# Kernel optimization log

Hardware: AMD Instinct MI355X
Metric: run time of the kernel (lower is better)

The kernel has to match this reference:

```python
import jax, jax.numpy as jnp
import numpy as np

D_MODEL = 1024
N_HEADS = 16
HEAD_DIM = D_MODEL // N_HEADS


def setup_inputs() -> dict:
    key = jax.random.key(0)
    ks = jax.random.split(key, 9)
    s = 1.0 / np.sqrt(D_MODEL)
    x = jax.random.normal(ks[0], (2, 2048, D_MODEL), dtype=jnp.float32)
    wq = jax.random.uniform(ks[1], (D_MODEL, D_MODEL), jnp.float32, -s, s)
    bq = jax.random.uniform(ks[2], (D_MODEL,), jnp.float32, -s, s)
    wk = jax.random.uniform(ks[3], (D_MODEL, D_MODEL), jnp.float32, -s, s)
    bk = jax.random.uniform(ks[4], (D_MODEL,), jnp.float32, -s, s)
    wv = jax.random.uniform(ks[5], (D_MODEL, D_MODEL), jnp.float32, -s, s)
    bv = jax.random.uniform(ks[6], (D_MODEL,), jnp.float32, -s, s)
    wo = jax.random.uniform(ks[7], (D_MODEL, D_MODEL), jnp.float32, -s, s)
    bo = jax.random.uniform(ks[8], (D_MODEL,), jnp.float32, -s, s)
    return {"x": x, "wq": wq, "bq": bq, "wk": wk, "bk": bk,
            "wv": wv, "bv": bv, "wo": wo, "bo": bo}


def reference(x, wq, bq, wk, bk, wv, bv, wo, bo):
    B, S, _ = x.shape
    scale = HEAD_DIM ** -0.5

    def proj(w, b):
        # torch Linear: x @ W^T + b, then split heads -> [B, H, S, Dh]
        y = jnp.einsum('bsd,ed->bse', x, w) + b
        return y.reshape(B, S, N_HEADS, HEAD_DIM).transpose(0, 2, 1, 3)

    q = proj(wq, bq)
    k = proj(wk, bk)
    v = proj(wv, bv)

    attn = jnp.einsum('bhqd,bhkd->bhqk', q, k) * scale  # [B,H,S,S]
    causal = jnp.triu(jnp.ones((S, S), dtype=bool), k=1)
    attn = jnp.where(causal, -jnp.inf, attn)
    attn = jax.nn.softmax(attn, axis=-1)
    out = jnp.einsum('bhqk,bhkd->bhqd', attn, v)
    out = out.transpose(0, 2, 1, 3).reshape(B, S, D_MODEL)
    return jnp.einsum('bsd,ed->bse', out, wo) + bo
```

## Files before the change

kernel.cpp:

```cpp
#include <hip/hip_runtime.h>
#include <hip/hip_bf16.h>

#define D_MODEL 1024
#define NHEADS  16
#define HDIM    64
#define SEQ     2048
#define BATCH   2
#define MROWS   (BATCH * SEQ)
#define CHELEM  ((size_t)BATCH * NHEADS * SEQ * HDIM)

typedef __bf16 bf16x8 __attribute__((ext_vector_type(8)));
typedef float  f32x4  __attribute__((ext_vector_type(4)));

__device__ __forceinline__ unsigned short f2bf(float f) {
  unsigned u = __builtin_bit_cast(unsigned, f);
  return (unsigned short)((u + 0x7fffu + ((u >> 16) & 1u)) >> 16);
}

__device__ __forceinline__ float fexp2(float x) {
#if __has_builtin(__builtin_amdgcn_exp2f)
  return __builtin_amdgcn_exp2f(x);
#else
  return __expf(x * 0.6931471805599453f);
#endif
}

__device__ __forceinline__ f32x4 mfma16(bf16x8 a, bf16x8 b, f32x4 c) {
  return __builtin_amdgcn_mfma_f32_16x16x32_bf16(a, b, c, 0, 0, 0);
}

__device__ __forceinline__ void gll16(const unsigned short* g, unsigned short* l) {
  __builtin_amdgcn_global_load_lds(
      (const __attribute__((address_space(1))) unsigned*)g,
      (__attribute__((address_space(3))) unsigned*)l, 16, 0, 0);
}

__global__ void cvt_f32_bf16(const float* __restrict__ in,
                             unsigned short* __restrict__ out, int n4) {
  int i = blockIdx.x * blockDim.x + threadIdx.x;
  if (i >= n4) return;
  float4 v = reinterpret_cast<const float4*>(in)[i];
  ushort4 o;
  o.x = f2bf(v.x); o.y = f2bf(v.y); o.z = f2bf(v.z); o.w = f2bf(v.w);
  reinterpret_cast<ushort4*>(out)[i] = o;
}

__global__ void cvt_w4(const float* __restrict__ s0, const float* __restrict__ s1,
                       const float* __restrict__ s2, const float* __restrict__ s3,
                       unsigned short* __restrict__ d0, unsigned short* __restrict__ d1,
                       unsigned short* __restrict__ d2, unsigned short* __restrict__ d3) {
  int i = blockIdx.x * blockDim.x + threadIdx.x;
  const int y = blockIdx.y;
  const float* s = (y == 0) ? s0 : (y == 1) ? s1 : (y == 2) ? s2 : s3;
  unsigned short* d = (y == 0) ? d0 : (y == 1) ? d1 : (y == 2) ? d2 : d3;
  float4 v = reinterpret_cast<const float4*>(s)[i];
  ushort4 o;
  o.x = f2bf(v.x); o.y = f2bf(v.y); o.z = f2bf(v.z); o.w = f2bf(v.w);
  reinterpret_cast<ushort4*>(d)[i] = o;
}

template <int MODE>
__global__ __launch_bounds__(256) void gemm_bt2(
    const unsigned short* __restrict__ A,
    const unsigned short* __restrict__ Bt,
    const float* __restrict__ b0, const float* __restrict__ b1,
    const float* __restrict__ b2,
    void* __restrict__ outp, int M, int N, int K) {
  __shared__ __align__(16) unsigned short lA[128 * 32];
  __shared__ __align__(16) unsigned short lB[128 * 32];
  const int tid = threadIdx.x;
  const int m0 = blockIdx.y * 128, n0 = blockIdx.x * 128;
  const int lane = tid & 63, wid = tid >> 6;
  const int wr = wid >> 1, wc = wid & 1;
  const int fr = lane & 15, g = lane >> 4;

  const int srow = wid * 32 + (lane >> 2);
  const int scol = (lane & 3) * 8;
  const unsigned short* gA = A + (size_t)(m0 + srow) * K + scol;
  const unsigned short* gB = Bt + (size_t)(n0 + srow) * K + scol;
  unsigned short* lAw = lA + wid * 1024;
  unsigned short* lBw = lB + wid * 1024;

  f32x4 acc[4][4];
#pragma unroll
  for (int i = 0; i < 4; ++i)
#pragma unroll
    for (int j = 0; j < 4; ++j) acc[i][j] = (f32x4){0.f, 0.f, 0.f, 0.f};

  for (int kt = 0; kt < K; kt += 32) {
    gll16(gA + kt, lAw);
    gll16(gA + (size_t)16 * K + kt, lAw + 512);
    gll16(gB + kt, lBw);
    gll16(gB + (size_t)16 * K + kt, lBw + 512);
    __syncthreads();
    bf16x8 af[4], bfv[4];
#pragma unroll
    for (int i = 0; i < 4; ++i)
      af[i] = *reinterpret_cast<const bf16x8*>(
          &lA[(wr * 64 + i * 16 + fr) * 32 + g * 8]);
#pragma unroll
    for (int j = 0; j < 4; ++j)
      bfv[j] = *reinterpret_cast<const bf16x8*>(
          &lB[(wc * 64 + j * 16 + fr) * 32 + g * 8]);
#pragma unroll
    for (int i = 0; i < 4; ++i)
#pragma unroll
      for (int j = 0; j < 4; ++j)
        acc[i][j] = mfma16(af[i], bfv[j], acc[i][j]);
    __syncthreads();
  }

  const int src = n0 >> 10;
  const float* bp = (MODE == 2) ? b0 : (src == 0 ? b0 : (src == 1 ? b1 : b2));
#pragma unroll
  for (int i = 0; i < 4; ++i)
#pragma unroll
    for (int j = 0; j < 4; ++j)
#pragma unroll
      for (int r = 0; r < 4; ++r) {
        int m = m0 + wr * 64 + i * 16 + g * 4 + r;
        int n = n0 + wc * 64 + j * 16 + fr;
        if (MODE == 2) {
          float val = acc[i][j][r] + bp[n];
          reinterpret_cast<float*>(outp)[(size_t)m * N + n] = val;
        } else {
          int within = n & 1023;
          float val = acc[i][j][r] + bp[within];
          if (src == 0) val *= 0.1803368867f;
          int b = m >> 11, s = m & 2047;
          int hh = within >> 6, dh = within & 63;
          size_t idx;
          if (src != 2)
            idx = ((size_t)(b * NHEADS + hh) * SEQ + s) * HDIM + dh;
          else
            idx = ((size_t)(b * NHEADS + hh) * HDIM + dh) * SEQ + s;
          reinterpret_cast<unsigned short*>(outp)[(size_t)src * CHELEM + idx] =
              f2bf(val);
        }
      }
}

__global__ __launch_bounds__(256) void attn_fwd10(
    const unsigned short* __restrict__ Q,
    const unsigned short* __restrict__ Km,
    const unsigned short* __restrict__ Vt,
    unsigned short* __restrict__ O) {
  const int tid = threadIdx.x;
  const int lane = tid & 63, wid = tid >> 6;
  const int fr = lane & 15, g = lane >> 4;
  const int lin = blockIdx.x;
  const int c = lin & 7;
  const int t = lin >> 3;
  const int j = t & 15;
  const int sgrp = t >> 4;
  const int slab = sgrp * 8 + c;
  const int b = slab >> 4, h = slab & 15;
  const int bh = b * NHEADS + h;

  __shared__ __align__(16) unsigned short lK[2][4096];
  __shared__ __align__(16) unsigned short lV[2][4096];
  __shared__ __align__(16) char plf[4][16 * 272];
  char* plw = plf[wid];

  const unsigned short* kptr = Km + (size_t)bh * SEQ * HDIM;
  const unsigned short* vptr = Vt + (size_t)bh * HDIM * SEQ;

  const int sr0 = tid >> 3;
  const int sch = tid & 7;
  const int schx = ((sch ^ (sr0 & 7)) << 3);
  const int kswz0 = ((g ^ (fr & 7)) << 3);
  const int kswz1 = (((4 + g) ^ (fr & 7)) << 3);

#define STAGE(BI, N0)                                                       \
  { gll16(kptr + (size_t)((N0) + sr0) * HDIM + schx, &lK[BI][wid * 512]);   \
    gll16(kptr + (size_t)((N0) + sr0 + 32) * HDIM + schx,                   \
          &lK[BI][2048 + wid * 512]);                                       \
    gll16(vptr + (size_t)sr0 * SEQ + (N0) + schx, &lV[BI][wid * 512]);      \
    gll16(vptr + (size_t)(sr0 + 32) * SEQ + (N0) + schx,                    \
          &lV[BI][2048 + wid * 512]); }

#pragma unroll 1
  for (int pass = 0; pass < 2; ++pass) {
    const int qt = pass ? (124 - 4 * j + wid) : (4 * j + wid);
    const int q0 = qt * 16;
    const int nkt = pass ? (32 - j) : (j + 1);

    const unsigned short* qb = Q + ((size_t)bh * SEQ + q0 + fr) * HDIM + g * 8;
    bf16x8 qa0 = *reinterpret_cast<const bf16x8*>(qb);
    bf16x8 qa1 = *reinterpret_cast<const bf16x8*>(qb + 32);

    f32x4 oacc[4];
#pragma unroll
    for (int i = 0; i < 4; ++i) oacc[i] = (f32x4){0.f, 0.f, 0.f, 0.f};
    float mreg[4] = {-3e30f, -3e30f, -3e30f, -3e30f};
    float lrow[4] = {0.f, 0.f, 0.f, 0.f};
    float mtile = -3e30f;

    STAGE(0, 0);
    __syncthreads();

    for (int kt = 0; kt < nkt; ++kt) {
      const int bi = kt & 1;
      if (kt + 1 < nkt) STAGE(bi ^ 1, (kt + 1) * 64);
      const int n0 = kt * 64;
      bf16x8 kf0[4], kf1[4];
#pragma unroll
      for (int cc = 0; cc < 4; ++cc) {
        kf0[cc] = *reinterpret_cast<const bf16x8*>(
            &lK[bi][(cc * 16 + fr) * 64 + kswz0]);
        kf1[cc] = *reinterpret_cast<const bf16x8*>(
            &lK[bi][(cc * 16 + fr) * 64 + kswz1]);
      }
      f32x4 s[4];
#pragma unroll
      for (int cc = 0; cc < 4; ++cc) {
        s[cc] = (f32x4){0.f, 0.f, 0.f, 0.f};
        s[cc] = mfma16(qa0, kf0[cc], s[cc]);
        s[cc] = mfma16(qa1, kf1[cc], s[cc]);
      }
      float sv[4][4];
      float lmax = -3e30f;
      if (kt == nkt - 1) {
#pragma unroll
        for (int cc = 0; cc < 4; ++cc)
#pragma unroll
          for (int r = 0; r < 4; ++r) {
            sv[cc][r] = (n0 + cc * 16 + fr <= q0 + g * 4 + r) ? s[cc][r]
                                                              : -1e30f;
            lmax = fmaxf(lmax, sv[cc][r]);
          }
      } else {
#pragma unroll
        for (int cc = 0; cc < 4; ++cc)
#pragma unroll
          for (int r = 0; r < 4; ++r) {
            sv[cc][r] = s[cc][r];
            lmax = fmaxf(lmax, sv[cc][r]);
          }
      }
      if (!__all(lmax - mtile <= 11.5f)) {
#pragma unroll
        for (int r = 0; r < 4; ++r) {
          float tm = fmaxf(fmaxf(sv[0][r], sv[1][r]), fmaxf(sv[2][r], sv[3][r]));
#pragma unroll
          for (int msk = 1; msk < 16; msk <<= 1)
            tm = fmaxf(tm, __shfl_xor(tm, msk, 64));
          const float mn = fmaxf(mreg[r], tm);
          const float al = fexp2(mreg[r] - mn);
          mreg[r] = mn;
          lrow[r] *= al;
#pragma unroll
          for (int nf = 0; nf < 4; ++nf) oacc[nf][r] *= al;
        }
        mtile = fminf(fminf(mreg[0], mreg[1]), fminf(mreg[2], mreg[3]));
      }
#pragma unroll
      for (int r = 0; r < 4; ++r) {
        const int rl = g * 4 + r;
#pragma unroll
        for (int cc = 0; cc < 4; ++cc) {
          float p = fexp2(sv[cc][r] - mreg[r]);
          lrow[r] += p;
          *reinterpret_cast<float*>(plw + rl * 272 + (cc * 16 + fr) * 4) = p;
        }
      }
#pragma unroll
      for (int blk = 0; blk < 2; ++blk) {
        const int abase = fr * 272 + blk * 128 + g * 32;
        f32x4 lo = *reinterpret_cast<const f32x4*>(plw + abase);
        f32x4 hi = *reinterpret_cast<const f32x4*>(plw + abase + 16);
        union { __bf16 e[8]; bf16x8 v; } cu;
#pragma unroll
        for (int t2 = 0; t2 < 4; ++t2) {
          cu.e[t2] = (__bf16)lo[t2];
          cu.e[4 + t2] = (__bf16)hi[t2];
        }
        bf16x8 pa = cu.v;
        const int vs = blk ? kswz1 : kswz0;
#pragma unroll
        for (int nf = 0; nf < 4; ++nf) {
          bf16x8 vfr = *reinterpret_cast<const bf16x8*>(
              &lV[bi][(nf * 16 + fr) * 64 + vs]);
          oacc[nf] = mfma16(pa, vfr, oacc[nf]);
        }
      }
      __syncthreads();
    }

#pragma unroll
    for (int r = 0; r < 4; ++r) {
      float ls = lrow[r];
#pragma unroll
      for (int msk = 1; msk < 16; msk <<= 1) ls += __shfl_xor(ls, msk, 64);
      const float inv = 1.f / ls;
      const size_t base =
          ((size_t)b * SEQ + q0 + g * 4 + r) * D_MODEL + h * HDIM;
#pragma unroll
      for (int nf = 0; nf < 4; ++nf)
        O[base + nf * 16 + fr] = f2bf(oacc[nf][r] * inv);
    }
  }
#undef STAGE
}

extern "C" void kernel_launch(void* const* d_in, const int* in_sizes, int n_in,
                              void* d_out, int out_size, void* d_ws,
                              size_t ws_size, hipStream_t stream) {
  const float* x  = (const float*)d_in[0];
  const float* wq = (const float*)d_in[1];
  const float* bq = (const float*)d_in[2];
  const float* wk = (const float*)d_in[3];
  const float* bk = (const float*)d_in[4];
  const float* wv = (const float*)d_in[5];
  const float* bv = (const float*)d_in[6];
  const float* wo = (const float*)d_in[7];
  const float* bo = (const float*)d_in[8];
  float* out = (float*)d_out;

  char* w = (char*)d_ws;
  unsigned short* xb    = (unsigned short*)w; w += (size_t)MROWS * D_MODEL * 2;
  unsigned short* wqkvb = (unsigned short*)w; w += (size_t)3 * D_MODEL * D_MODEL * 2;
  unsigned short* wob   = (unsigned short*)w; w += (size_t)D_MODEL * D_MODEL * 2;
  unsigned short* Qb    = (unsigned short*)w; w += CHELEM * 2 * 3;
  unsigned short* Ob    = (unsigned short*)w; w += (size_t)MROWS * D_MODEL * 2;
  unsigned short* Kb  = Qb + CHELEM;
  unsigned short* Vtb = Qb + 2 * CHELEM;

  {
    int n4 = MROWS * D_MODEL / 4;
    cvt_f32_bf16<<<n4 / 256, 256, 0, stream>>>(x, xb, n4);
  }
  {
    int n4 = D_MODEL * D_MODEL / 4;
    cvt_w4<<<dim3(n4 / 256, 4), 256, 0, stream>>>(
        wq, wk, wv, wo, wqkvb, wqkvb + (size_t)D_MODEL * D_MODEL,
        wqkvb + (size_t)2 * D_MODEL * D_MODEL, wob);
  }

  gemm_bt2<3><<<dim3(3 * D_MODEL / 128, MROWS / 128), 256, 0, stream>>>(
      xb, wqkvb, bq, bk, bv, Qb, MROWS, 3 * D_MODEL, D_MODEL);

  attn_fwd10<<<512, 256, 0, stream>>>(Qb, Kb, Vtb, Ob);

  gemm_bt2<2><<<dim3(D_MODEL / 128, MROWS / 128), 256, 0, stream>>>(
      Ob, wob, bo, bo, bo, out, MROWS, D_MODEL, D_MODEL);
}
```

Before: 132.5 us.

## Fuse both causal query passes into one KV sweep and store P as bf16

The two sequential passes over K/V, one for an early query tile and one for the mirrored late tile, become a single loop. Both tiles share each staged K/V block, so the early tile's K/V blocks are loaded once instead of twice. V fragments are hoisted into registers and reused by both tiles. The probability scratch now holds swizzled bf16 instead of padded fp32, which shrinks LDS traffic and drops the repacking conversion. The cost is roughly double the accumulator and softmax register state, which may lower occupancy or cause spills.

```diff
diff --git a/kernel.cpp b/kernel.cpp
--- a/kernel.cpp
+++ b/kernel.cpp
@@ -140,7 +140,7 @@
       }
 }
 
-__global__ __launch_bounds__(256) void attn_fwd10(
+__global__ __launch_bounds__(256) void attn_fwd11(
     const unsigned short* __restrict__ Q,
     const unsigned short* __restrict__ Km,
     const unsigned short* __restrict__ Vt,
@@ -159,8 +159,10 @@
 
   __shared__ __align__(16) unsigned short lK[2][4096];
   __shared__ __align__(16) unsigned short lV[2][4096];
-  __shared__ __align__(16) char plf[4][16 * 272];
-  char* plw = plf[wid];
+  __shared__ __align__(16) unsigned short plA[4][1024];
+  __shared__ __align__(16) unsigned short plB[4][1024];
+  char* plwA = reinterpret_cast<char*>(plA[wid]);
+  char* plwB = reinterpret_cast<char*>(plB[wid]);
 
   const unsigned short* kptr = Km + (size_t)bh * SEQ * HDIM;
   const unsigned short* vptr = Vt + (size_t)bh * HDIM * SEQ;
@@ -179,128 +181,141 @@
     gll16(vptr + (size_t)(sr0 + 32) * SEQ + (N0) + schx,                    \
           &lV[BI][2048 + wid * 512]); }
 
-#pragma unroll 1
-  for (int pass = 0; pass < 2; ++pass) {
-    const int qt = pass ? (124 - 4 * j + wid) : (4 * j + wid);
-    const int q0 = qt * 16;
-    const int nkt = pass ? (32 - j) : (j + 1);
-
-    const unsigned short* qb = Q + ((size_t)bh * SEQ + q0 + fr) * HDIM + g * 8;
-    bf16x8 qa0 = *reinterpret_cast<const bf16x8*>(qb);
-    bf16x8 qa1 = *reinterpret_cast<const bf16x8*>(qb + 32);
-
-    f32x4 oacc[4];
-#pragma unroll
-    for (int i = 0; i < 4; ++i) oacc[i] = (f32x4){0.f, 0.f, 0.f, 0.f};
-    float mreg[4] = {-3e30f, -3e30f, -3e30f, -3e30f};
-    float lrow[4] = {0.f, 0.f, 0.f, 0.f};
-    float mtile = -3e30f;
-
-    STAGE(0, 0);
+#define QKSTEP(QA0, QA1, S)                                                 \
+  { _Pragma("unroll") for (int cc = 0; cc < 4; ++cc) {                      \
+      S[cc] = (f32x4){0.f, 0.f, 0.f, 0.f};                                  \
+      S[cc] = mfma16(QA0, kf0[cc], S[cc]);                                  \
+      S[cc] = mfma16(QA1, kf1[cc], S[cc]);                                  \
+    } }
+
+#define SMAXP(S, MREG, LROW, OACC, MTILE, PLW, Q0, ISLAST, N0)              \
+  { float sv[4][4];                                                         \
+    float lmax = -3e30f;                                                    \
+    if (ISLAST) {                                                           \
+      _Pragma("unroll") for (int cc = 0; cc < 4; ++cc)                      \
+      _Pragma("unroll") for (int r = 0; r < 4; ++r) {                       \
+        sv[cc][r] = ((N0) + cc * 16 + fr <= (Q0) + g * 4 + r) ? S[cc][r]    \
+                                                              : -1e30f;     \
+        lmax = fmaxf(lmax, sv[cc][r]);                                      \
+      }                                                                     \
+    } else {                                                                \
+      _Pragma("unroll") for (int cc = 0; cc < 4; ++cc)                      \
+      _Pragma("unroll") for (int r = 0; r < 4; ++r) {                       \
+        sv[cc][r] = S[cc][r];                                               \
+        lmax = fmaxf(lmax, sv[cc][r]);                                      \
+      }                                                                     \
+    }                                                                       \
+    if (!__all(lmax - MTILE <= 11.5f)) {                                    \
+      _Pragma("unroll") for (int r = 0; r < 4; ++r) {                       \
+        float tm = fmaxf(fmaxf(sv[0][r], sv[1][r]),                         \
+                         fmaxf(sv[2][r], sv[3][r]));                        \
+        _Pragma("unroll") for (int msk = 1; msk < 16; msk <<= 1)            \
+            tm = fmaxf(tm, __shfl_xor(tm, msk, 64));                        \
+        const float mn = fmaxf(MREG[r], tm);                                \
+        const float al = fexp2(MREG[r] - mn);                               \
+        MREG[r] = mn;                                                       \
+        LROW[r] *= al;                                                      \
+        _Pragma("unroll") for (int nf = 0; nf < 4; ++nf)                    \
+            OACC[nf][r] *= al;                                              \
+      }                                                                     \
+      MTILE = fminf(fminf(MREG[0], MREG[1]), fminf(MREG[2], MREG[3]));      \
+    }                                                                       \
+    _Pragma("unroll") for (int r = 0; r < 4; ++r) {                         \
+      const int rl = g * 4 + r;                                             \
+      _Pragma("unroll") for (int cc = 0; cc < 4; ++cc) {                    \
+        float p = fexp2(sv[cc][r] - MREG[r]);                               \
+        LROW[r] += p;                                                       \
+        int byte = (rl * 128 + (cc * 16 + fr) * 2) ^ ((rl & 7) << 4);       \
+        *reinterpret_cast<unsigned short*>((PLW) + byte) =                  \
+            __builtin_bit_cast(unsigned short, (__bf16)p);                  \
+      }                                                                     \
+    } }
+
+#define PVSTEP(PLW, OACC)                                                   \
+  { _Pragma("unroll") for (int blk = 0; blk < 2; ++blk) {                   \
+      int byte = (fr * 128 + blk * 64 + g * 16) ^ ((fr & 7) << 4);          \
+      bf16x8 pa = *reinterpret_cast<const bf16x8*>((PLW) + byte);           \
+      _Pragma("unroll") for (int nf = 0; nf < 4; ++nf)                      \
+          OACC[nf] = mfma16(pa, vfr[blk][nf], OACC[nf]);                    \
+    } }
+
+#define EPI(LROW, OACC, Q0)                                                 \
+  { _Pragma("unroll") for (int r = 0; r < 4; ++r) {                         \
+      float ls = LROW[r];                                                   \
+      _Pragma("unroll") for (int msk = 1; msk < 16; msk <<= 1)              \
+          ls += __shfl_xor(ls, msk, 64);                                    \
+      const float inv = 1.f / ls;                                           \
+      const size_t base =                                                   \
+          ((size_t)b * SEQ + (Q0) + g * 4 + r) * D_MODEL + h * HDIM;        \
+      _Pragma("unroll") for (int nf = 0; nf < 4; ++nf)                      \
+          O[base + nf * 16 + fr] = f2bf(OACC[nf][r] * inv);                 \
+    } }
+
+  const int qtA = 4 * j + wid, q0A = qtA * 16, nktA = j + 1;
+  const int qtB = 124 - 4 * j + wid, q0B = qtB * 16, nktB = 32 - j;
+
+  const unsigned short* qbA = Q + ((size_t)bh * SEQ + q0A + fr) * HDIM + g * 8;
+  bf16x8 qaA0 = *reinterpret_cast<const bf16x8*>(qbA);
+  bf16x8 qaA1 = *reinterpret_cast<const bf16x8*>(qbA + 32);
+  const unsigned short* qbB = Q + ((size_t)bh * SEQ + q0B + fr) * HDIM + g * 8;
+  bf16x8 qaB0 = *reinterpret_cast<const bf16x8*>(qbB);
+  bf16x8 qaB1 = *reinterpret_cast<const bf16x8*>(qbB + 32);
+
+  f32x4 oaccA[4], oaccB[4];
+#pragma unroll
+  for (int i = 0; i < 4; ++i) {
+    oaccA[i] = (f32x4){0.f, 0.f, 0.f, 0.f};
+    oaccB[i] = (f32x4){0.f, 0.f, 0.f, 0.f};
+  }
+  float mregA[4] = {-3e30f, -3e30f, -3e30f, -3e30f};
+  float mregB[4] = {-3e30f, -3e30f, -3e30f, -3e30f};
+  float lrowA[4] = {0.f, 0.f, 0.f, 0.f};
+  float lrowB[4] = {0.f, 0.f, 0.f, 0.f};
+  float mtileA = -3e30f, mtileB = -3e30f;
+
+  STAGE(0, 0);
+  __syncthreads();
+
+  for (int kt = 0; kt < nktB; ++kt) {
+    const int bi = kt & 1;
+    if (kt + 1 < nktB) STAGE(bi ^ 1, (kt + 1) * 64);
+    const int n0 = kt * 64;
+    bf16x8 kf0[4], kf1[4];
+#pragma unroll
+    for (int cc = 0; cc < 4; ++cc) {
+      kf0[cc] = *reinterpret_cast<const bf16x8*>(
+          &lK[bi][(cc * 16 + fr) * 64 + kswz0]);
+      kf1[cc] = *reinterpret_cast<const bf16x8*>(
+          &lK[bi][(cc * 16 + fr) * 64 + kswz1]);
+    }
+    bf16x8 vfr[2][4];
+#pragma unroll
+    for (int blk = 0; blk < 2; ++blk) {
+      const int vs = blk ? kswz1 : kswz0;
+#pragma unroll
+      for (int nf = 0; nf < 4; ++nf)
+        vfr[blk][nf] = *reinterpret_cast<const bf16x8*>(
+            &lV[bi][(nf * 16 + fr) * 64 + vs]);
+    }
+    const bool actA = (kt < nktA);
+    f32x4 sA[4], sB[4];
+    if (actA) QKSTEP(qaA0, qaA1, sA);
+    QKSTEP(qaB0, qaB1, sB);
+    if (actA) SMAXP(sA, mregA, lrowA, oaccA, mtileA, plwA, q0A,
+                    kt == nktA - 1, n0);
+    SMAXP(sB, mregB, lrowB, oaccB, mtileB, plwB, q0B, kt == nktB - 1, n0);
+    if (actA) PVSTEP(plwA, oaccA);
+    PVSTEP(plwB, oaccB);
     __syncthreads();
-
-    for (int kt = 0; kt < nkt; ++kt) {
-      const int bi = kt & 1;
-      if (kt + 1 < nkt) STAGE(bi ^ 1, (kt + 1) * 64);
-      const int n0 = kt * 64;
-      bf16x8 kf0[4], kf1[4];
-#pragma unroll
-      for (int cc = 0; cc < 4; ++cc) {
-        kf0[cc] = *reinterpret_cast<const bf16x8*>(
-            &lK[bi][(cc * 16 + fr) * 64 + kswz0]);
-        kf1[cc] = *reinterpret_cast<const bf16x8*>(
-            &lK[bi][(cc * 16 + fr) * 64 + kswz1]);
-      }
-      f32x4 s[4];
-#pragma unroll
-      for (int cc = 0; cc < 4; ++cc) {
-        s[cc] = (f32x4){0.f, 0.f, 0.f, 0.f};
-        s[cc] = mfma16(qa0, kf0[cc], s[cc]);
-        s[cc] = mfma16(qa1, kf1[cc], s[cc]);
-      }
-      float sv[4][4];
-      float lmax = -3e30f;
-      if (kt == nkt - 1) {
-#pragma unroll
-        for (int cc = 0; cc < 4; ++cc)
-#pragma unroll
-          for (int r = 0; r < 4; ++r) {
-            sv[cc][r] = (n0 + cc * 16 + fr <= q0 + g * 4 + r) ? s[cc][r]
-                                                              : -1e30f;
-            lmax = fmaxf(lmax, sv[cc][r]);
-          }
-      } else {
-#pragma unroll
-        for (int cc = 0; cc < 4; ++cc)
-#pragma unroll
-          for (int r = 0; r < 4; ++r) {
-            sv[cc][r] = s[cc][r];
-            lmax = fmaxf(lmax, sv[cc][r]);
-          }
-      }
-      if (!__all(lmax - mtile <= 11.5f)) {
-#pragma unroll
-        for (int r = 0; r < 4; ++r) {
-          float tm = fmaxf(fmaxf(sv[0][r], sv[1][r]), fmaxf(sv[2][r], sv[3][r]));
-#pragma unroll
-          for (int msk = 1; msk < 16; msk <<= 1)
-            tm = fmaxf(tm, __shfl_xor(tm, msk, 64));
-          const float mn = fmaxf(mreg[r], tm);
-          const float al = fexp2(mreg[r] - mn);
-          mreg[r] = mn;
-          lrow[r] *= al;
-#pragma unroll
-          for (int nf = 0; nf < 4; ++nf) oacc[nf][r] *= al;
-        }
-        mtile = fminf(fminf(mreg[0], mreg[1]), fminf(mreg[2], mreg[3]));
-      }
-#pragma unroll
-      for (int r = 0; r < 4; ++r) {
-        const int rl = g * 4 + r;
-#pragma unroll
-        for (int cc = 0; cc < 4; ++cc) {
-          float p = fexp2(sv[cc][r] - mreg[r]);
-          lrow[r] += p;
-          *reinterpret_cast<float*>(plw + rl * 272 + (cc * 16 + fr) * 4) = p;
-        }
-      }
-#pragma unroll
-      for (int blk = 0; blk < 2; ++blk) {
-        const int abase = fr * 272 + blk * 128 + g * 32;
-        f32x4 lo = *reinterpret_cast<const f32x4*>(plw + abase);
-        f32x4 hi = *reinterpret_cast<const f32x4*>(plw + abase + 16);
-        union { __bf16 e[8]; bf16x8 v; } cu;
-#pragma unroll
-        for (int t2 = 0; t2 < 4; ++t2) {
-          cu.e[t2] = (__bf16)lo[t2];
-          cu.e[4 + t2] = (__bf16)hi[t2];
-        }
-        bf16x8 pa = cu.v;
-        const int vs = blk ? kswz1 : kswz0;
-#pragma unroll
-        for (int nf = 0; nf < 4; ++nf) {
-          bf16x8 vfr = *reinterpret_cast<const bf16x8*>(
-              &lV[bi][(nf * 16 + fr) * 64 + vs]);
-          oacc[nf] = mfma16(pa, vfr, oacc[nf]);
-        }
-      }
-      __syncthreads();
-    }
-
-#pragma unroll
-    for (int r = 0; r < 4; ++r) {
-      float ls = lrow[r];
-#pragma unroll
-      for (int msk = 1; msk < 16; msk <<= 1) ls += __shfl_xor(ls, msk, 64);
-      const float inv = 1.f / ls;
-      const size_t base =
-          ((size_t)b * SEQ + q0 + g * 4 + r) * D_MODEL + h * HDIM;
-#pragma unroll
-      for (int nf = 0; nf < 4; ++nf)
-        O[base + nf * 16 + fr] = f2bf(oacc[nf][r] * inv);
-    }
-  }
+  }
+
+  EPI(lrowA, oaccA, q0A);
+  EPI(lrowB, oaccB, q0B);
 #undef STAGE
+#undef QKSTEP
+#undef SMAXP
+#undef PVSTEP
+#undef EPI
 }
 
 extern "C" void kernel_launch(void* const* d_in, const int* in_sizes, int n_in,
@@ -340,7 +355,7 @@
   gemm_bt2<3><<<dim3(3 * D_MODEL / 128, MROWS / 128), 256, 0, stream>>>(
       xb, wqkvb, bq, bk, bv, Qb, MROWS, 3 * D_MODEL, D_MODEL);
 
-  attn_fwd10<<<512, 256, 0, stream>>>(Qb, Kb, Vtb, Ob);
+  attn_fwd11<<<512, 256, 0, stream>>>(Qb, Kb, Vtb, Ob);
 
   gemm_bt2<2><<<dim3(D_MODEL / 128, MROWS / 128), 256, 0, stream>>>(
       Ob, wob, bo, bo, bo, out, MROWS, D_MODEL, D_MODEL);
```

Result: slower. 136.1 us (+2.7%).

## Compute transposed S tiles so P stays in registers for the PV MFMA

Applied to the files above, without the earlier changes.

Swaps the MFMA operand order so each lane holds the scores for a single query row across keys. Softmax probabilities can then be packed straight into bf16 MFMA operands, with no LDS round-trip through a per-wave P buffer. Row max and sum reductions shrink to two cross-group shuffles, and the output is written as 4-element vector stores. The cost is that V fragments are now assembled from two 8-byte LDS reads per operand, and the layout change increases the risk of swizzle or indexing mistakes.

```diff
diff --git a/kernel.cpp b/kernel.cpp
--- a/kernel.cpp
+++ b/kernel.cpp
@@ -140,7 +140,7 @@
       }
 }
 
-__global__ __launch_bounds__(256) void attn_fwd10(
+__global__ __launch_bounds__(256) void attn_fwd12(
     const unsigned short* __restrict__ Q,
     const unsigned short* __restrict__ Km,
     const unsigned short* __restrict__ Vt,
@@ -159,8 +159,6 @@
 
   __shared__ __align__(16) unsigned short lK[2][4096];
   __shared__ __align__(16) unsigned short lV[2][4096];
-  __shared__ __align__(16) char plf[4][16 * 272];
-  char* plw = plf[wid];
 
   const unsigned short* kptr = Km + (size_t)bh * SEQ * HDIM;
   const unsigned short* vptr = Vt + (size_t)bh * HDIM * SEQ;
@@ -170,6 +168,11 @@
   const int schx = ((sch ^ (sr0 & 7)) << 3);
   const int kswz0 = ((g ^ (fr & 7)) << 3);
   const int kswz1 = (((4 + g) ^ (fr & 7)) << 3);
+  const int g2 = g >> 1, gh = (g & 1) * 4;
+  const int vlo0 = (((0 + g2) ^ (fr & 7)) << 3) + gh;
+  const int vhi0 = (((2 + g2) ^ (fr & 7)) << 3) + gh;
+  const int vlo1 = (((4 + g2) ^ (fr & 7)) << 3) + gh;
+  const int vhi1 = (((6 + g2) ^ (fr & 7)) << 3) + gh;
 
 #define STAGE(BI, N0)                                                       \
   { gll16(kptr + (size_t)((N0) + sr0) * HDIM + schx, &lK[BI][wid * 512]);   \
@@ -184,17 +187,17 @@
     const int qt = pass ? (124 - 4 * j + wid) : (4 * j + wid);
     const int q0 = qt * 16;
     const int nkt = pass ? (32 - j) : (j + 1);
-
-    const unsigned short* qb = Q + ((size_t)bh * SEQ + q0 + fr) * HDIM + g * 8;
+    const int qg = q0 + fr;
+
+    const unsigned short* qb = Q + ((size_t)bh * SEQ + qg) * HDIM + g * 8;
     bf16x8 qa0 = *reinterpret_cast<const bf16x8*>(qb);
     bf16x8 qa1 = *reinterpret_cast<const bf16x8*>(qb + 32);
 
     f32x4 oacc[4];
 #pragma unroll
     for (int i = 0; i < 4; ++i) oacc[i] = (f32x4){0.f, 0.f, 0.f, 0.f};
-    float mreg[4] = {-3e30f, -3e30f, -3e30f, -3e30f};
-    float lrow[4] = {0.f, 0.f, 0.f, 0.f};
-    float mtile = -3e30f;
+    float mreg = -3e30f;
+    float lrow = 0.f;
 
     STAGE(0, 0);
     __syncthreads();
@@ -215,8 +218,8 @@
 #pragma unroll
       for (int cc = 0; cc < 4; ++cc) {
         s[cc] = (f32x4){0.f, 0.f, 0.f, 0.f};
-        s[cc] = mfma16(qa0, kf0[cc], s[cc]);
-        s[cc] = mfma16(qa1, kf1[cc], s[cc]);
+        s[cc] = mfma16(kf0[cc], qa0, s[cc]);
+        s[cc] = mfma16(kf1[cc], qa1, s[cc]);
       }
       float sv[4][4];
       float lmax = -3e30f;
@@ -225,8 +228,8 @@
         for (int cc = 0; cc < 4; ++cc)
 #pragma unroll
           for (int r = 0; r < 4; ++r) {
-            sv[cc][r] = (n0 + cc * 16 + fr <= q0 + g * 4 + r) ? s[cc][r]
-                                                              : -1e30f;
+            sv[cc][r] =
+                (n0 + cc * 16 + g * 4 + r <= qg) ? s[cc][r] : -1e30f;
             lmax = fmaxf(lmax, sv[cc][r]);
           }
       } else {
@@ -238,66 +241,55 @@
             lmax = fmaxf(lmax, sv[cc][r]);
           }
       }
-      if (!__all(lmax - mtile <= 11.5f)) {
-#pragma unroll
-        for (int r = 0; r < 4; ++r) {
-          float tm = fmaxf(fmaxf(sv[0][r], sv[1][r]), fmaxf(sv[2][r], sv[3][r]));
-#pragma unroll
-          for (int msk = 1; msk < 16; msk <<= 1)
-            tm = fmaxf(tm, __shfl_xor(tm, msk, 64));
-          const float mn = fmaxf(mreg[r], tm);
-          const float al = fexp2(mreg[r] - mn);
-          mreg[r] = mn;
-          lrow[r] *= al;
-#pragma unroll
-          for (int nf = 0; nf < 4; ++nf) oacc[nf][r] *= al;
-        }
-        mtile = fminf(fminf(mreg[0], mreg[1]), fminf(mreg[2], mreg[3]));
-      }
+      if (!__all(lmax - mreg <= 11.5f)) {
+        float tm = lmax;
+        tm = fmaxf(tm, __shfl_xor(tm, 16, 64));
+        tm = fmaxf(tm, __shfl_xor(tm, 32, 64));
+        const float mn = fmaxf(mreg, tm);
+        const float al = fexp2(mreg - mn);
+        mreg = mn;
+        lrow *= al;
+#pragma unroll
+        for (int nf = 0; nf < 4; ++nf) oacc[nf] *= al;
+      }
+      union { __bf16 e[8]; bf16x8 v; } pk0, pk1;
 #pragma unroll
       for (int r = 0; r < 4; ++r) {
-        const int rl = g * 4 + r;
-#pragma unroll
-        for (int cc = 0; cc < 4; ++cc) {
-          float p = fexp2(sv[cc][r] - mreg[r]);
-          lrow[r] += p;
-          *reinterpret_cast<float*>(plw + rl * 272 + (cc * 16 + fr) * 4) = p;
-        }
-      }
-#pragma unroll
-      for (int blk = 0; blk < 2; ++blk) {
-        const int abase = fr * 272 + blk * 128 + g * 32;
-        f32x4 lo = *reinterpret_cast<const f32x4*>(plw + abase);
-        f32x4 hi = *reinterpret_cast<const f32x4*>(plw + abase + 16);
-        union { __bf16 e[8]; bf16x8 v; } cu;
-#pragma unroll
-        for (int t2 = 0; t2 < 4; ++t2) {
-          cu.e[t2] = (__bf16)lo[t2];
-          cu.e[4 + t2] = (__bf16)hi[t2];
-        }
-        bf16x8 pa = cu.v;
-        const int vs = blk ? kswz1 : kswz0;
-#pragma unroll
-        for (int nf = 0; nf < 4; ++nf) {
-          bf16x8 vfr = *reinterpret_cast<const bf16x8*>(
-              &lV[bi][(nf * 16 + fr) * 64 + vs]);
-          oacc[nf] = mfma16(pa, vfr, oacc[nf]);
-        }
+        float p0 = fexp2(sv[0][r] - mreg);
+        float p1 = fexp2(sv[1][r] - mreg);
+        float p2 = fexp2(sv[2][r] - mreg);
+        float p3 = fexp2(sv[3][r] - mreg);
+        lrow += (p0 + p1) + (p2 + p3);
+        pk0.e[r] = (__bf16)p0; pk0.e[4 + r] = (__bf16)p1;
+        pk1.e[r] = (__bf16)p2; pk1.e[4 + r] = (__bf16)p3;
+      }
+#pragma unroll
+      for (int nf = 0; nf < 4; ++nf) {
+        const int vrow = (nf * 16 + fr) * 64;
+        union { unsigned long long d[2]; bf16x8 v; } v0, v1;
+        v0.d[0] = *reinterpret_cast<const unsigned long long*>(&lV[bi][vrow + vlo0]);
+        v0.d[1] = *reinterpret_cast<const unsigned long long*>(&lV[bi][vrow + vhi0]);
+        v1.d[0] = *reinterpret_cast<const unsigned long long*>(&lV[bi][vrow + vlo1]);
+        v1.d[1] = *reinterpret_cast<const unsigned long long*>(&lV[bi][vrow + vhi1]);
+        oacc[nf] = mfma16(v0.v, pk0.v, oacc[nf]);
+        oacc[nf] = mfma16(v1.v, pk1.v, oacc[nf]);
       }
       __syncthreads();
     }
 
-#pragma unroll
-    for (int r = 0; r < 4; ++r) {
-      float ls = lrow[r];
-#pragma unroll
-      for (int msk = 1; msk < 16; msk <<= 1) ls += __shfl_xor(ls, msk, 64);
-      const float inv = 1.f / ls;
-      const size_t base =
-          ((size_t)b * SEQ + q0 + g * 4 + r) * D_MODEL + h * HDIM;
-#pragma unroll
-      for (int nf = 0; nf < 4; ++nf)
-        O[base + nf * 16 + fr] = f2bf(oacc[nf][r] * inv);
+    float ls = lrow;
+    ls += __shfl_xor(ls, 16, 64);
+    ls += __shfl_xor(ls, 32, 64);
+    const float inv = 1.f / ls;
+    const size_t obase = ((size_t)b * SEQ + qg) * D_MODEL + h * HDIM + g * 4;
+#pragma unroll
+    for (int nf = 0; nf < 4; ++nf) {
+      ushort4 o4;
+      o4.x = f2bf(oacc[nf][0] * inv);
+      o4.y = f2bf(oacc[nf][1] * inv);
+      o4.z = f2bf(oacc[nf][2] * inv);
+      o4.w = f2bf(oacc[nf][3] * inv);
+      *reinterpret_cast<ushort4*>(&O[obase + nf * 16]) = o4;
     }
   }
 #undef STAGE
@@ -340,7 +332,7 @@
   gemm_bt2<3><<<dim3(3 * D_MODEL / 128, MROWS / 128), 256, 0, stream>>>(
       xb, wqkvb, bq, bk, bv, Qb, MROWS, 3 * D_MODEL, D_MODEL);
 
-  attn_fwd10<<<512, 256, 0, stream>>>(Qb, Kb, Vtb, Ob);
+  attn_fwd12<<<512, 256, 0, stream>>>(Qb, Kb, Vtb, Ob);
 
   gemm_bt2<2><<<dim3(D_MODEL / 128, MROWS / 128), 256, 0, stream>>>(
       Ob, wob, bo, bo, bo, out, MROWS, D_MODEL, D_MODEL);
```

Result: faster. 128.4 us (-3.1%).
